# Performance work log

Measured on AMD Instinct MI355X. Metric: run time of the kernel, lower is better.

## Reference

```python
import jax, jax.numpy as jnp
import numpy as np

RING_SIZES = list(range(3, 27, 2))  # 3,5,...,25 -> 12 rings; (1+12)*96 = 1248
BN_EPS = 1e-5


def _box_sum(x, k):
    """Sum over k x k window (k odd), 'same' zero padding. x: [B,C,H,W].
    O(1) per pixel via summed-area table instead of dense depthwise conv."""
    p = k // 2
    H, W = x.shape[2], x.shape[3]
    xp = jnp.pad(x, ((0, 0), (0, 0), (p, p), (p, p)))
    S = jnp.cumsum(jnp.cumsum(xp, axis=2), axis=3)
    S = jnp.pad(S, ((0, 0), (0, 0), (1, 0), (1, 0)))  # leading zero row/col
    return (S[:, :, k:k + H, k:k + W] - S[:, :, :H, k:k + W]
            - S[:, :, k:k + H, :W] + S[:, :, :H, :W])


def _ring_sum(x, k):
    """Depthwise conv with a k x k ring of ones == box(k) - box(k-2)."""
    inner = x if k == 3 else _box_sum(x, k - 2)
    return _box_sum(x, k) - inner


def _bn_eval(x, gamma, beta, mean, var):
    scale = gamma / jnp.sqrt(var + BN_EPS)
    return x * scale[None, :, None, None] + (beta - mean * scale)[None, :, None, None]


def _conv1x1(x, w, b):
    # x: [B,C,H,W], w: [O,C] -> [B,O,H,W]
    return jnp.einsum('bchw,oc->bohw', x, w) + b[None, :, None, None]


def setup_inputs() -> dict:
    key = jax.random.key(0)
    ks = jax.random.split(key, 13)
    B, C, H, W = 4, 96, 128, 128
    return {
        'x': jax.random.normal(ks[0], (B, C, H, W), jnp.float32),
        'bn1_gamma': jax.random.uniform(ks[1], (1248,), jnp.float32, 0.5, 1.5),
        'bn1_beta': jax.random.normal(ks[2], (1248,), jnp.float32) * 0.1,
        'bn1_mean': jax.random.normal(ks[3], (1248,), jnp.float32),
        'bn1_var': jax.random.uniform(ks[4], (1248,), jnp.float32, 0.5, 1.5),
        'conv1_w': jax.random.normal(ks[5], (512, 1248), jnp.float32) * (1.0 / np.sqrt(1248)),
        'conv1_b': jax.random.normal(ks[6], (512,), jnp.float32) * 0.01,
        'bn2_gamma': jax.random.uniform(ks[7], (512,), jnp.float32, 0.5, 1.5),
        'bn2_beta': jax.random.normal(ks[8], (512,), jnp.float32) * 0.1,
        'bn2_mean': jax.random.normal(ks[9], (512,), jnp.float32),
        'bn2_var': jax.random.uniform(ks[10], (512,), jnp.float32, 0.5, 1.5),
        'conv2_w': jax.random.normal(ks[11], (96, 512), jnp.float32) * (1.0 / np.sqrt(512)),
        'conv2_b': jax.random.normal(ks[12], (96,), jnp.float32) * 0.01,
    }


def reference(x, bn1_gamma, bn1_beta, bn1_mean, bn1_var, conv1_w, conv1_b,
              bn2_gamma, bn2_beta, bn2_mean, bn2_var, conv2_w, conv2_b):
    convs = [x] + [_ring_sum(x, k) for k in RING_SIZES]
    h = jnp.concatenate(convs, axis=1)  # [B, 1248, H, W]
    h = _bn_eval(h, bn1_gamma, bn1_beta, bn1_mean, bn1_var)
    h = jax.nn.relu(_conv1x1(h, conv1_w, conv1_b))
    h = _bn_eval(h, bn2_gamma, bn2_beta, bn2_mean, bn2_var)
    return _conv1x1(h, conv2_w, conv2_b)
```

## Files before the change

### kernel.cpp

```cpp
#include <hip/hip_runtime.h>
#include <hip/hip_bf16.h>
#include <cstdint>

typedef __attribute__((ext_vector_type(8))) short bf16x8;
typedef __attribute__((ext_vector_type(4))) float f32x4;

#define BN_EPS 1e-5f

__global__ __launch_bounds__(256) void prep1_kernel(
    const float* __restrict__ W1, const float* __restrict__ cb1,
    const float* __restrict__ g1, const float* __restrict__ be1,
    const float* __restrict__ mu1, const float* __restrict__ va1,
    __hip_bfloat16* __restrict__ V, float* __restrict__ b1e)
{
  int o = blockIdx.x;
  int t = threadIdx.x;
  const float* wrow = W1 + (size_t)o * 1248;
  float acc = 0.f;
  for (int i = t; i < 1248; i += 256) {
    float s = g1[i] * rsqrtf(va1[i] + BN_EPS);
    float w = wrow[i];
    acc += w * (be1[i] - mu1[i] * s);
    float g = w * s;
    float gn = 0.f;
    if (i < 1152) {
      float sn = g1[i + 96] * rsqrtf(va1[i + 96] + BN_EPS);
      gn = wrow[i + 96] * sn;
    }
    V[(size_t)o * 1248 + i] = __float2bfloat16(g - gn);
  }
  for (int d = 32; d > 0; d >>= 1) acc += __shfl_down(acc, d);
  __shared__ float red[4];
  int lane = t & 63, wv = t >> 6;
  if (lane == 0) red[wv] = acc;
  __syncthreads();
  if (t == 0) b1e[o] = cb1[o] + red[0] + red[1] + red[2] + red[3];
}

__global__ __launch_bounds__(256) void prep2_kernel(
    const float* __restrict__ W2, const float* __restrict__ cb2,
    const float* __restrict__ g2, const float* __restrict__ be2,
    const float* __restrict__ mu2, const float* __restrict__ va2,
    __hip_bfloat16* __restrict__ W2e, float* __restrict__ b2e)
{
  int o = blockIdx.x;
  int t = threadIdx.x;
  const float* wrow = W2 + (size_t)o * 512;
  float acc = 0.f;
  for (int j = t; j < 512; j += 256) {
    float s = g2[j] * rsqrtf(va2[j] + BN_EPS);
    float wv = wrow[j];
    acc += wv * (be2[j] - mu2[j] * s);
    W2e[(size_t)o * 512 + j] = __float2bfloat16(wv * s);
  }
  for (int d = 32; d > 0; d >>= 1) acc += __shfl_down(acc, d);
  __shared__ float red[4];
  int lane = t & 63, wv2 = t >> 6;
  if (lane == 0) red[wv2] = acc;
  __syncthreads();
  if (t == 0) b2e[o] = cb2[o] + red[0] + red[1] + red[2] + red[3];
}

__global__ __launch_bounds__(128) void sat_kernel(
    const float* __restrict__ x, float* __restrict__ SAT)
{
  int plane = blockIdx.x;
  const float* xp = x + (size_t)plane * 16384;
  __shared__ float tile[16384];
  int t = threadIdx.x;
  for (int i4 = t; i4 < 4096; i4 += 128) {
    int r = i4 >> 5;
    int g = i4 & 31;
    float4 v = *(const float4*)(xp + (size_t)r * 128 + g * 4);
    *(float4*)(tile + r * 128 + ((g ^ (r & 31)) << 2)) = v;
  }
  __syncthreads();
  {
    int r = t;
    float carry = 0.f;
    for (int g = 0; g < 32; ++g) {
      float* p = tile + r * 128 + ((g ^ (r & 31)) << 2);
      float4 v = *(float4*)p;
      float s0 = carry + v.x, s1 = s0 + v.y, s2 = s1 + v.z, s3 = s2 + v.w;
      float4 o; o.x = s0; o.y = s1; o.z = s2; o.w = s3;
      *(float4*)p = o;
      carry = s3;
    }
  }
  __syncthreads();
  float* Sg = SAT + (size_t)plane * 17028;
  Sg[t] = 0.f;
  if (t < 4) Sg[128 + t] = 0.f;
  Sg[(t + 1) * 132] = 0.f;
  int gc = t >> 2, wc = t & 3;
  float run = 0.f;
  for (int r = 0; r < 128; ++r) {
    run += tile[r * 128 + ((gc ^ (r & 31)) << 2) + wc];
    Sg[(r + 1) * 132 + t + 1] = run;
  }
}

__global__ __launch_bounds__(512, 2) void fused1_kernel(
    const float* __restrict__ SAT, const __hip_bfloat16* __restrict__ V,
    const float* __restrict__ b1e, __hip_bfloat16* __restrict__ Y1, int nb)
{
  extern __shared__ __align__(16) char smem[];
  float* E = (float*)smem;
  __hip_bfloat16* As = (__hip_bfloat16*)(smem + 50688);

  int blk = blockIdx.x;
  int rows_per_xcd = (nb * 128) >> 3;
  int r = (blk & 7) * rows_per_xcd + (blk >> 3);
  int bL = r >> 7, y = r & 127;

  int t = threadIdx.x;
  int lane = t & 63, wv = t >> 6;
  int lr = lane & 15, quad = lane >> 4;
  int px = t & 127;
  int bg = t >> 7;

  const float* Sb = SAT + (size_t)bL * 96 * 17028;

  f32x4 acc[8][4];
#pragma unroll
  for (int i = 0; i < 8; ++i)
#pragma unroll
    for (int jn = 0; jn < 4; ++jn) acc[i][jn] = (f32x4){0.f, 0.f, 0.f, 0.f};

  auto efill = [&](int j) {
    int y1 = (y - j < 0) ? 0 : (y - j);
    int y2 = ((y + j > 127) ? 127 : (y + j)) + 1;
    for (int idx = t; idx < 3168; idx += 512) {
      int cl = idx / 33;
      int ck = idx - cl * 33;
      const float* bp = Sb + (size_t)cl * 17028 + ck * 4;
      float4 a = *(const float4*)(bp + y2 * 132);
      float4 b = *(const float4*)(bp + y1 * 132);
      float4 d;
      d.x = a.x - b.x; d.y = a.y - b.y; d.z = a.z - b.z; d.w = a.w - b.w;
      *(float4*)(E + cl * 132 + ck * 4) = d;
    }
  };

  efill(0);
  __syncthreads();

  for (int j = 0; j < 13; ++j) {
    int x1 = (px - j < 0) ? 0 : (px - j);
    int x2 = ((px + j > 127) ? 127 : (px + j)) + 1;
#pragma unroll
    for (int pass = 0; pass < 3; ++pass) {
      int g = bg + pass * 4;
      const float* Eb = E + g * 8 * 132;
      union { bf16x8 v; __hip_bfloat16 h[8]; } pk;
#pragma unroll
      for (int i = 0; i < 8; ++i)
        pk.h[i] = __float2bfloat16(Eb[i * 132 + x2] - Eb[i * 132 + x1]);
      *(bf16x8*)(As + px * 104 + g * 8) = pk.v;
    }
    __syncthreads();

#pragma unroll
    for (int sub = 0; sub < 3; ++sub) {
      bf16x8 af[8], bfr[4];
#pragma unroll
      for (int i = 0; i < 8; ++i)
        af[i] = *(const bf16x8*)(As + (i * 16 + lr) * 104 + sub * 32 + quad * 8);
#pragma unroll
      for (int jn = 0; jn < 4; ++jn)
        bfr[jn] = *(const bf16x8*)(V + (size_t)(wv * 64 + jn * 16 + lr) * 1248
                                   + j * 96 + sub * 32 + quad * 8);
#pragma unroll
      for (int i = 0; i < 8; ++i)
#pragma unroll
        for (int jn = 0; jn < 4; ++jn)
          acc[i][jn] = __builtin_amdgcn_mfma_f32_16x16x32_bf16(af[i], bfr[jn], acc[i][jn], 0, 0, 0);
      if (sub == 0 && j < 12) efill(j + 1);
    }
    __syncthreads();
  }

  size_t mrow = (size_t)bL * 16384 + (size_t)y * 128;
  __hip_bfloat16* Yst = (__hip_bfloat16*)smem;
#pragma unroll
  for (int half = 0; half < 2; ++half) {
    if ((wv >> 2) == half) {
      __hip_bfloat16* st = Yst + (size_t)(wv & 3) * (128 * 64);
#pragma unroll
      for (int jn = 0; jn < 4; ++jn) {
        int n = wv * 64 + jn * 16 + lr;
        float bias = b1e[n];
#pragma unroll
        for (int i = 0; i < 8; ++i) {
#pragma unroll
          for (int rr = 0; rr < 4; ++rr) {
            int m = i * 16 + quad * 4 + rr;
            float z = acc[i][jn][rr] + bias;
            z = z > 0.f ? z : 0.f;
            st[m * 64 + jn * 16 + lr] = __float2bfloat16(z);
          }
        }
      }
    }
    __syncthreads();
#pragma unroll
    for (int it = 0; it < 8; ++it) {
      int q = it * 512 + t;
      int p2 = q >> 5, ck = q & 31;
      uint4 v = *(uint4*)(Yst + (size_t)(ck >> 3) * (128 * 64) + p2 * 64 + (ck & 7) * 8);
      *(uint4*)(Y1 + (mrow + p2) * 512 + half * 256 + ck * 8) = v;
    }
    __syncthreads();
  }
}

__global__ __launch_bounds__(256) void gemm2_kernel(
    const __hip_bfloat16* __restrict__ Y1,
    const __hip_bfloat16* __restrict__ W2e,
    const float* __restrict__ b2e,
    float* __restrict__ out, int b0)
{
  int lane = threadIdx.x & 63, wv = threadIdx.x >> 6;
  int lr = lane & 15, quad = lane >> 4;
  int pw = blockIdx.x * 256 + wv * 64;

  f32x4 acc[6][4];
#pragma unroll
  for (int im = 0; im < 6; ++im)
#pragma unroll
    for (int jn = 0; jn < 4; ++jn) acc[im][jn] = (f32x4){0.f, 0.f, 0.f, 0.f};

  for (int k0 = 0; k0 < 512; k0 += 32) {
    bf16x8 bfrag[4], afrag[6];
#pragma unroll
    for (int jn = 0; jn < 4; ++jn)
      bfrag[jn] = *(const bf16x8*)(Y1 + (size_t)(pw + jn * 16 + lr) * 512 + k0 + quad * 8);
#pragma unroll
    for (int im = 0; im < 6; ++im)
      afrag[im] = *(const bf16x8*)(W2e + (size_t)(im * 16 + lr) * 512 + k0 + quad * 8);
#pragma unroll
    for (int im = 0; im < 6; ++im)
#pragma unroll
      for (int jn = 0; jn < 4; ++jn)
        acc[im][jn] = __builtin_amdgcn_mfma_f32_16x16x32_bf16(afrag[im], bfrag[jn], acc[im][jn], 0, 0, 0);
  }

#pragma unroll
  for (int im = 0; im < 6; ++im) {
#pragma unroll
    for (int r = 0; r < 4; ++r) {
      int o2 = im * 16 + quad * 4 + r;
      float bias = b2e[o2];
#pragma unroll
      for (int jn = 0; jn < 4; ++jn) {
        int p = pw + jn * 16 + lr;
        out[((size_t)(b0 + (p >> 14)) * 96 + o2) * 16384 + (p & 16383)] =
            acc[im][jn][r] + bias;
      }
    }
  }
}

extern "C" void kernel_launch(void* const* d_in, const int* in_sizes, int n_in,
                              void* d_out, int out_size, void* d_ws, size_t ws_size,
                              hipStream_t stream)
{
  const float* x   = (const float*)d_in[0];
  const float* g1  = (const float*)d_in[1];
  const float* be1 = (const float*)d_in[2];
  const float* mu1 = (const float*)d_in[3];
  const float* va1 = (const float*)d_in[4];
  const float* W1  = (const float*)d_in[5];
  const float* cb1 = (const float*)d_in[6];
  const float* g2  = (const float*)d_in[7];
  const float* be2 = (const float*)d_in[8];
  const float* mu2 = (const float*)d_in[9];
  const float* va2 = (const float*)d_in[10];
  const float* W2  = (const float*)d_in[11];
  const float* cb2 = (const float*)d_in[12];
  float* out = (float*)d_out;

  hipFuncSetAttribute((const void*)fused1_kernel,
                      hipFuncAttributeMaxDynamicSharedMemorySize, 77312);

  char* w = (char*)d_ws;
  __hip_bfloat16* V   = (__hip_bfloat16*)w; w += (size_t)512 * 1248 * 2;
  __hip_bfloat16* W2e = (__hip_bfloat16*)w; w += (size_t)96 * 512 * 2;
  float* b1e = (float*)w; w += 2048;
  float* b2e = (float*)w; w += 512;
  size_t fixed = (size_t)(w - (char*)d_ws);

  const size_t satB = (size_t)96 * 17028 * 4;
  const size_t yB   = (size_t)16384 * 512 * 2;
  int nb = (ws_size >= fixed + 4 * (satB + yB) + 4096) ? 4 : 1;

  float* SAT = (float*)w; w += (size_t)nb * satB;
  w = (char*)(((uintptr_t)w + 255) & ~(uintptr_t)255);
  __hip_bfloat16* Y1 = (__hip_bfloat16*)w;

  prep1_kernel<<<512, 256, 0, stream>>>(W1, cb1, g1, be1, mu1, va1, V, b1e);
  prep2_kernel<<<96, 256, 0, stream>>>(W2, cb2, g2, be2, mu2, va2, W2e, b2e);

  for (int b0 = 0; b0 < 4; b0 += nb) {
    sat_kernel<<<nb * 96, 128, 0, stream>>>(x + (size_t)b0 * 96 * 16384, SAT);
    fused1_kernel<<<nb * 128, 512, 77312, stream>>>(SAT, V, b1e, Y1, nb);
    gemm2_kernel<<<nb * 64, 256, 0, stream>>>(Y1, W2e, b2e, out, b0);
  }
}
```

Baseline: 309.7 us.

## Fuse second 1x1 GEMM into first fused kernel, drop Y1 round-trip

Folds the second pointwise GEMM (512->96) into the ring-sum/GEMM1 kernel. Each block now keeps its 128x512 ReLU'd bf16 activation row in shared memory and computes the output directly, so the Y1 intermediate no longer goes to global memory and there is no separate gemm2 launch. Block size grows to 1024 threads with a 2x8 wave tiling of GEMM1, and shared memory grows to 133 KB. In exchange, only one block fits per CU, each wave holds half as many accumulators, and the small GEMM2 phase runs serially after GEMM1 inside each block.

```diff
diff --git a/kernel.cpp b/kernel.cpp
--- a/kernel.cpp
+++ b/kernel.cpp
@@ -100,9 +100,10 @@
   }
 }
 
-__global__ __launch_bounds__(512, 2) void fused1_kernel(
+__global__ __launch_bounds__(1024) void fused1_kernel(
     const float* __restrict__ SAT, const __hip_bfloat16* __restrict__ V,
-    const float* __restrict__ b1e, __hip_bfloat16* __restrict__ Y1, int nb)
+    const float* __restrict__ b1e, const __hip_bfloat16* __restrict__ W2e,
+    const float* __restrict__ b2e, float* __restrict__ out, int nb, int b0)
 {
   extern __shared__ __align__(16) char smem[];
   float* E = (float*)smem;
@@ -115,22 +116,23 @@
 
   int t = threadIdx.x;
   int lane = t & 63, wv = t >> 6;
+  int wm = wv & 1, wn = wv >> 1;
   int lr = lane & 15, quad = lane >> 4;
   int px = t & 127;
   int bg = t >> 7;
 
   const float* Sb = SAT + (size_t)bL * 96 * 17028;
 
-  f32x4 acc[8][4];
-#pragma unroll
-  for (int i = 0; i < 8; ++i)
+  f32x4 acc[4][4];
+#pragma unroll
+  for (int i = 0; i < 4; ++i)
 #pragma unroll
     for (int jn = 0; jn < 4; ++jn) acc[i][jn] = (f32x4){0.f, 0.f, 0.f, 0.f};
 
   auto efill = [&](int j) {
     int y1 = (y - j < 0) ? 0 : (y - j);
     int y2 = ((y + j > 127) ? 127 : (y + j)) + 1;
-    for (int idx = t; idx < 3168; idx += 512) {
+    for (int idx = t; idx < 3168; idx += 1024) {
       int cl = idx / 33;
       int ck = idx - cl * 33;
       const float* bp = Sb + (size_t)cl * 17028 + ck * 4;
@@ -148,30 +150,36 @@
   for (int j = 0; j < 13; ++j) {
     int x1 = (px - j < 0) ? 0 : (px - j);
     int x2 = ((px + j > 127) ? 127 : (px + j)) + 1;
-#pragma unroll
-    for (int pass = 0; pass < 3; ++pass) {
-      int g = bg + pass * 4;
-      const float* Eb = E + g * 8 * 132;
+    {
+      const float* Eb = E + bg * 8 * 132;
       union { bf16x8 v; __hip_bfloat16 h[8]; } pk;
 #pragma unroll
       for (int i = 0; i < 8; ++i)
         pk.h[i] = __float2bfloat16(Eb[i * 132 + x2] - Eb[i * 132 + x1]);
-      *(bf16x8*)(As + px * 104 + g * 8) = pk.v;
+      *(bf16x8*)(As + px * 104 + bg * 8) = pk.v;
+      if (bg < 4) {
+        const float* Eb2 = E + (8 + bg) * 8 * 132;
+        union { bf16x8 v; __hip_bfloat16 h[8]; } pk2;
+#pragma unroll
+        for (int i = 0; i < 8; ++i)
+          pk2.h[i] = __float2bfloat16(Eb2[i * 132 + x2] - Eb2[i * 132 + x1]);
+        *(bf16x8*)(As + px * 104 + (8 + bg) * 8) = pk2.v;
+      }
     }
     __syncthreads();
 
 #pragma unroll
     for (int sub = 0; sub < 3; ++sub) {
-      bf16x8 af[8], bfr[4];
-#pragma unroll
-      for (int i = 0; i < 8; ++i)
-        af[i] = *(const bf16x8*)(As + (i * 16 + lr) * 104 + sub * 32 + quad * 8);
+      bf16x8 af[4], bfr[4];
+#pragma unroll
+      for (int i = 0; i < 4; ++i)
+        af[i] = *(const bf16x8*)(As + (wm * 64 + i * 16 + lr) * 104 + sub * 32 + quad * 8);
 #pragma unroll
       for (int jn = 0; jn < 4; ++jn)
-        bfr[jn] = *(const bf16x8*)(V + (size_t)(wv * 64 + jn * 16 + lr) * 1248
+        bfr[jn] = *(const bf16x8*)(V + (size_t)(wn * 64 + jn * 16 + lr) * 1248
                                    + j * 96 + sub * 32 + quad * 8);
 #pragma unroll
-      for (int i = 0; i < 8; ++i)
+      for (int i = 0; i < 4; ++i)
 #pragma unroll
         for (int jn = 0; jn < 4; ++jn)
           acc[i][jn] = __builtin_amdgcn_mfma_f32_16x16x32_bf16(af[i], bfr[jn], acc[i][jn], 0, 0, 0);
@@ -180,83 +188,47 @@
     __syncthreads();
   }
 
-  size_t mrow = (size_t)bL * 16384 + (size_t)y * 128;
   __hip_bfloat16* Yst = (__hip_bfloat16*)smem;
 #pragma unroll
-  for (int half = 0; half < 2; ++half) {
-    if ((wv >> 2) == half) {
-      __hip_bfloat16* st = Yst + (size_t)(wv & 3) * (128 * 64);
-#pragma unroll
-      for (int jn = 0; jn < 4; ++jn) {
-        int n = wv * 64 + jn * 16 + lr;
-        float bias = b1e[n];
-#pragma unroll
-        for (int i = 0; i < 8; ++i) {
-#pragma unroll
-          for (int rr = 0; rr < 4; ++rr) {
-            int m = i * 16 + quad * 4 + rr;
-            float z = acc[i][jn][rr] + bias;
-            z = z > 0.f ? z : 0.f;
-            st[m * 64 + jn * 16 + lr] = __float2bfloat16(z);
-          }
-        }
+  for (int jn = 0; jn < 4; ++jn) {
+    int n = wn * 64 + jn * 16 + lr;
+    float bias = b1e[n];
+#pragma unroll
+    for (int i = 0; i < 4; ++i) {
+#pragma unroll
+      for (int rr = 0; rr < 4; ++rr) {
+        int m = wm * 64 + i * 16 + quad * 4 + rr;
+        float z = acc[i][jn][rr] + bias;
+        z = z > 0.f ? z : 0.f;
+        Yst[m * 520 + n] = __float2bfloat16(z);
       }
     }
-    __syncthreads();
-#pragma unroll
-    for (int it = 0; it < 8; ++it) {
-      int q = it * 512 + t;
-      int p2 = q >> 5, ck = q & 31;
-      uint4 v = *(uint4*)(Yst + (size_t)(ck >> 3) * (128 * 64) + p2 * 64 + (ck & 7) * 8);
-      *(uint4*)(Y1 + (mrow + p2) * 512 + half * 256 + ck * 8) = v;
-    }
-    __syncthreads();
-  }
-}
-
-__global__ __launch_bounds__(256) void gemm2_kernel(
-    const __hip_bfloat16* __restrict__ Y1,
-    const __hip_bfloat16* __restrict__ W2e,
-    const float* __restrict__ b2e,
-    float* __restrict__ out, int b0)
-{
-  int lane = threadIdx.x & 63, wv = threadIdx.x >> 6;
-  int lr = lane & 15, quad = lane >> 4;
-  int pw = blockIdx.x * 256 + wv * 64;
-
-  f32x4 acc[6][4];
-#pragma unroll
-  for (int im = 0; im < 6; ++im)
-#pragma unroll
-    for (int jn = 0; jn < 4; ++jn) acc[im][jn] = (f32x4){0.f, 0.f, 0.f, 0.f};
-
-  for (int k0 = 0; k0 < 512; k0 += 32) {
-    bf16x8 bfrag[4], afrag[6];
-#pragma unroll
-    for (int jn = 0; jn < 4; ++jn)
-      bfrag[jn] = *(const bf16x8*)(Y1 + (size_t)(pw + jn * 16 + lr) * 512 + k0 + quad * 8);
-#pragma unroll
-    for (int im = 0; im < 6; ++im)
-      afrag[im] = *(const bf16x8*)(W2e + (size_t)(im * 16 + lr) * 512 + k0 + quad * 8);
-#pragma unroll
-    for (int im = 0; im < 6; ++im)
-#pragma unroll
-      for (int jn = 0; jn < 4; ++jn)
-        acc[im][jn] = __builtin_amdgcn_mfma_f32_16x16x32_bf16(afrag[im], bfrag[jn], acc[im][jn], 0, 0, 0);
-  }
-
-#pragma unroll
-  for (int im = 0; im < 6; ++im) {
-#pragma unroll
-    for (int r = 0; r < 4; ++r) {
-      int o2 = im * 16 + quad * 4 + r;
-      float bias = b2e[o2];
-#pragma unroll
-      for (int jn = 0; jn < 4; ++jn) {
-        int p = pw + jn * 16 + lr;
-        out[((size_t)(b0 + (p >> 14)) * 96 + o2) * 16384 + (p & 16383)] =
-            acc[im][jn][r] + bias;
-      }
+  }
+  __syncthreads();
+
+  int pxt = wv & 7;
+  int mh = wv >> 3;
+  f32x4 acc2[3];
+#pragma unroll
+  for (int im = 0; im < 3; ++im) acc2[im] = (f32x4){0.f, 0.f, 0.f, 0.f};
+
+  for (int k2 = 0; k2 < 512; k2 += 32) {
+    bf16x8 bfr2 = *(const bf16x8*)(Yst + (pxt * 16 + lr) * 520 + k2 + quad * 8);
+#pragma unroll
+    for (int im = 0; im < 3; ++im) {
+      bf16x8 afr2 = *(const bf16x8*)(W2e + (size_t)(mh * 48 + im * 16 + lr) * 512
+                                     + k2 + quad * 8);
+      acc2[im] = __builtin_amdgcn_mfma_f32_16x16x32_bf16(afr2, bfr2, acc2[im], 0, 0, 0);
+    }
+  }
+
+  size_t obase = ((size_t)(b0 + bL) * 96) * 16384 + (size_t)y * 128 + pxt * 16 + lr;
+#pragma unroll
+  for (int im = 0; im < 3; ++im) {
+#pragma unroll
+    for (int rr = 0; rr < 4; ++rr) {
+      int o2 = mh * 48 + im * 16 + quad * 4 + rr;
+      out[obase + (size_t)o2 * 16384] = acc2[im][rr] + b2e[o2];
     }
   }
 }
@@ -281,7 +253,7 @@
   float* out = (float*)d_out;
 
   hipFuncSetAttribute((const void*)fused1_kernel,
-                      hipFuncAttributeMaxDynamicSharedMemorySize, 77312);
+                      hipFuncAttributeMaxDynamicSharedMemorySize, 133120);
 
   char* w = (char*)d_ws;
   __hip_bfloat16* V   = (__hip_bfloat16*)w; w += (size_t)512 * 1248 * 2;
@@ -291,19 +263,15 @@
   size_t fixed = (size_t)(w - (char*)d_ws);
 
   const size_t satB = (size_t)96 * 17028 * 4;
-  const size_t yB   = (size_t)16384 * 512 * 2;
-  int nb = (ws_size >= fixed + 4 * (satB + yB) + 4096) ? 4 : 1;
-
-  float* SAT = (float*)w; w += (size_t)nb * satB;
-  w = (char*)(((uintptr_t)w + 255) & ~(uintptr_t)255);
-  __hip_bfloat16* Y1 = (__hip_bfloat16*)w;
+  int nb = (ws_size >= fixed + 4 * satB + 4096) ? 4 : 1;
+
+  float* SAT = (float*)w;
 
   prep1_kernel<<<512, 256, 0, stream>>>(W1, cb1, g1, be1, mu1, va1, V, b1e);
   prep2_kernel<<<96, 256, 0, stream>>>(W2, cb2, g2, be2, mu2, va2, W2e, b2e);
 
   for (int b0 = 0; b0 < 4; b0 += nb) {
     sat_kernel<<<nb * 96, 128, 0, stream>>>(x + (size_t)b0 * 96 * 16384, SAT);
-    fused1_kernel<<<nb * 128, 512, 77312, stream>>>(SAT, V, b1e, Y1, nb);
-    gemm2_kernel<<<nb * 64, 256, 0, stream>>>(Y1, W2e, b2e, out, b0);
-  }
-}
+    fused1_kernel<<<nb * 128, 1024, 133120, stream>>>(SAT, V, b1e, W2e, b2e, out, nb, b0);
+  }
+}
```

New measurement: 302.2 us. 1.02x faster.
